# Kernel optimization log

Hardware: AMD Instinct MI355X
Metric: run time of the kernel (lower is better)

## Reference

```python
import jax, jax.numpy as jnp
import numpy as np

N_NODES = 100000


def gcn_conv(x, W, b, src, dst, n):
    """PyG GCNConv with default add_self_loops and symmetric normalization."""
    xw = x @ W  # [N, out]
    loop = jnp.arange(n, dtype=src.dtype)
    s = jnp.concatenate([src, loop])  # source j
    d = jnp.concatenate([dst, loop])  # target i
    deg = jax.ops.segment_sum(jnp.ones_like(d, dtype=xw.dtype), d, num_segments=n)
    dinv = jnp.where(deg > 0, jax.lax.rsqrt(deg), 0.0)
    norm = dinv[s] * dinv[d]  # [E+N]
    msg = xw[s] * norm[:, None]
    out = jax.ops.segment_sum(msg, d, num_segments=n)
    return out + b


def setup_inputs() -> dict:
    key = jax.random.key(0)
    ks = jax.random.split(key, 9)
    n, e, f = N_NODES, 1600000, 512
    x = jax.random.normal(ks[0], (n, f), dtype=jnp.float32)
    edge_index = jax.random.randint(ks[1], (2, e), 0, n, dtype=jnp.int32)
    y = jax.random.uniform(ks[2], (n, 1), dtype=jnp.float32)
    W1 = jax.random.normal(ks[3], (f, 64), dtype=jnp.float32) / np.sqrt(f)
    b1 = jnp.zeros((64,), jnp.float32)
    W2 = jax.random.normal(ks[4], (64, 256), dtype=jnp.float32) / np.sqrt(64)
    b2 = jnp.zeros((256,), jnp.float32)
    W3 = jax.random.normal(ks[5], (256, 1), dtype=jnp.float32) / np.sqrt(256)
    b3 = jnp.zeros((1,), jnp.float32)
    return {"x": x, "edge_index": edge_index, "y": y,
            "W1": W1, "b1": b1, "W2": W2, "b2": b2, "W3": W3, "b3": b3}


def reference(x, edge_index, y, W1, b1, W2, b2, W3, b3):
    n = x.shape[0]
    src, dst = edge_index[0], edge_index[1]
    h = jax.nn.relu(gcn_conv(x, W1, b1, src, dst, n))
    # dropout is identity in eval mode
    h = jax.nn.relu(gcn_conv(h, W2, b2, src, dst, n))
    z = gcn_conv(h, W3, b3, src, dst, n)  # logits [N, 1]
    # BCE(sigmoid(z), y), computed stably via log-sigmoid
    loss = -(y * jax.nn.log_sigmoid(z) + (1.0 - y) * jax.nn.log_sigmoid(-z))
    return jnp.mean(loss)
```

## Files before the change

### kernel.cpp

```cpp
#include <hip/hip_runtime.h>
#include <math.h>

typedef __attribute__((ext_vector_type(8))) short s16x8;
typedef __attribute__((ext_vector_type(4))) float f32x4;

__device__ inline ushort f2bf(float f) {
    union { float f; unsigned u; } v; v.f = f;
    unsigned r = v.u + 0x7FFF + ((v.u >> 16) & 1);
    return (ushort)(r >> 16);
}
__device__ inline float bf2f(ushort h) {
    union { unsigned u; float f; } v; v.u = ((unsigned)h) << 16;
    return v.f;
}
__device__ inline float bfLo(unsigned u) {
    union { unsigned x; float f; } v; v.x = u << 16; return v.f;
}
__device__ inline float bfHi(unsigned u) {
    union { unsigned x; float f; } v; v.x = u & 0xFFFF0000u; return v.f;
}


__global__ void hist_wsplit_kernel(const int* __restrict__ dst, int E, int eb,
                                   int* __restrict__ cnt8, int N, int* __restrict__ slot,
                                   const float* __restrict__ W1, const float* __restrict__ W2,
                                   ushort* __restrict__ wt_hi, ushort* __restrict__ wt_lo,
                                   ushort* __restrict__ wt2_hi, ushort* __restrict__ wt2_lo) {
    int b = blockIdx.x;
    if (b < eb) {
        int e = b * 256 + threadIdx.x;
        if (e < E) {
            int g = b & 7;
            slot[e] = atomicAdd(&cnt8[(size_t)g * N + dst[e]], 1);
        }
        return;
    }
    int idx = (b - eb) * 256 + threadIdx.x;
    if (idx < 64 * 512) {
        int n = idx & 63, k = idx >> 6;
        float f = W1[k * 64 + n];
        ushort h = f2bf(f);
        wt_hi[n * 512 + k] = h;
        wt_lo[n * 512 + k] = f2bf(f - bf2f(h));
    } else if (idx < 64 * 512 + 64 * 256) {
        int i2 = idx - 64 * 512;
        int n = i2 & 255, k = i2 >> 8;
        float f = W2[k * 256 + n];
        ushort h = f2bf(f);
        wt2_hi[n * 64 + k] = h;
        wt2_lo[n * 64 + k] = f2bf(f - bf2f(h));
    }
}

__global__ void alloc_kernel(const int* __restrict__ cnt8, int N,
                             int* __restrict__ row_start, int* __restrict__ base8,
                             int* __restrict__ deg, float* __restrict__ dinv,
                             int* __restrict__ total, float* __restrict__ out) {
    int i = blockIdx.x * blockDim.x + threadIdx.x;
    int lane = threadIdx.x & 63;
    int cg[8];
    int c = 0;
    if (i < N) {
#pragma unroll
        for (int g = 0; g < 8; g++) { cg[g] = cnt8[(size_t)g * N + i]; c += cg[g]; }
    } else {
#pragma unroll
        for (int g = 0; g < 8; g++) cg[g] = 0;
    }
    int inc = c;
#pragma unroll
    for (int o = 1; o < 64; o <<= 1) {
        int v = __shfl_up(inc, o, 64);
        if (lane >= o) inc += v;
    }
    int wsum = __shfl(inc, 63, 64);
    int base = 0;
    if (lane == 0) base = atomicAdd(total, wsum);
    base = __shfl(base, 0, 64);
    if (i < N) {
        int rs = base + inc - c;
        row_start[i] = rs;
        deg[i] = c;
        dinv[i] = rsqrtf((float)(c + 1));
        int run = rs;
#pragma unroll
        for (int g = 0; g < 8; g++) { base8[(size_t)g * N + i] = run; run += cg[g]; }
    }
    if (i == 0) *out = 0.f;
}

__global__ __launch_bounds__(256, 3) void gemm1_scatter_kernel(
        const float* __restrict__ x, const ushort* __restrict__ wt_hi,
        const ushort* __restrict__ wt_lo, const float* __restrict__ dinv,
        ushort* __restrict__ out, int N, int GB,
        const int* __restrict__ src, const int* __restrict__ dstp, int E,
        const int* __restrict__ base8, const int* __restrict__ slot,
        int* __restrict__ csr) {
    __shared__ __align__(16) short xs_hi[128 * 64];
    __shared__ __align__(16) short xs_lo[128 * 64];
    __shared__ __align__(16) short ws_hi[64 * 64];
    __shared__ __align__(16) short ws_lo[64 * 64];

    if ((int)blockIdx.x >= GB) {
        int sb = (int)blockIdx.x - GB;
        int e = sb * 256 + threadIdx.x;
        if (e < E) {
            int d = dstp[e];
            int g = sb & 7;
            csr[base8[(size_t)g * N + d] + slot[e]] = src[e];
        }
        return;
    }

    const int tid = threadIdx.x;
    const int nodeBase = blockIdx.x * 128;
    const int wave = tid >> 6, lane = tid & 63;
    const int m16 = lane & 15, quad = lane >> 4;

    f32x4 acc[2][4];
#pragma unroll
    for (int mt = 0; mt < 2; mt++)
#pragma unroll
        for (int nt = 0; nt < 4; nt++) acc[mt][nt] = (f32x4){0.f, 0.f, 0.f, 0.f};

    for (int kc = 0; kc < 512; kc += 64) {
        __syncthreads();
#pragma unroll
        for (int i = 0; i < 4; i++) {
            int f = tid + i * 256;
            int node = f >> 3, g = f & 7;
            int gn = nodeBase + node;
            if (gn >= N) gn = N - 1;
            const float4 a = *(const float4*)(x + (size_t)gn * 512 + kc + g * 8);
            const float4 b = *(const float4*)(x + (size_t)gn * 512 + kc + g * 8 + 4);
            float ff[8] = {a.x, a.y, a.z, a.w, b.x, b.y, b.z, b.w};
            union { ushort u[8]; uint4 v; } H, L;
#pragma unroll
            for (int j = 0; j < 8; j++) {
                ushort h = f2bf(ff[j]);
                H.u[j] = h;
                L.u[j] = f2bf(ff[j] - bf2f(h));
            }
            int gp = (g + node) & 7;
            *(uint4*)&xs_hi[node * 64 + gp * 8] = H.v;
            *(uint4*)&xs_lo[node * 64 + gp * 8] = L.v;
        }
#pragma unroll
        for (int i = 0; i < 2; i++) {
            int f = tid + i * 256;
            int n = f >> 3, g = f & 7;
            int gp = (g + n) & 7;
            *(uint4*)&ws_hi[n * 64 + gp * 8] =
                *(const uint4*)(wt_hi + (size_t)n * 512 + kc + g * 8);
            *(uint4*)&ws_lo[n * 64 + gp * 8] =
                *(const uint4*)(wt_lo + (size_t)n * 512 + kc + g * 8);
        }
        __syncthreads();
#pragma unroll
        for (int ck = 0; ck < 2; ck++) {
            s16x8 Ah[2], Al[2];
#pragma unroll
            for (int mt = 0; mt < 2; mt++) {
                int row = (wave * 2 + mt) * 16 + m16;
                int gp = (ck * 4 + quad + row) & 7;
                Ah[mt] = *(s16x8*)&xs_hi[row * 64 + gp * 8];
                Al[mt] = *(s16x8*)&xs_lo[row * 64 + gp * 8];
            }
#pragma unroll
            for (int nt = 0; nt < 4; nt++) {
                int n = nt * 16 + m16;
                int gp = (ck * 4 + quad + n) & 7;
                s16x8 Bh = *(s16x8*)&ws_hi[n * 64 + gp * 8];
                s16x8 Bl = *(s16x8*)&ws_lo[n * 64 + gp * 8];
#pragma unroll
                for (int mt = 0; mt < 2; mt++) {
                    acc[mt][nt] = __builtin_amdgcn_mfma_f32_16x16x32_bf16(Ah[mt], Bh, acc[mt][nt], 0, 0, 0);
                    acc[mt][nt] = __builtin_amdgcn_mfma_f32_16x16x32_bf16(Ah[mt], Bl, acc[mt][nt], 0, 0, 0);
                    acc[mt][nt] = __builtin_amdgcn_mfma_f32_16x16x32_bf16(Al[mt], Bh, acc[mt][nt], 0, 0, 0);
                }
            }
        }
    }
#pragma unroll
    for (int mt = 0; mt < 2; mt++) {
#pragma unroll
        for (int r = 0; r < 4; r++) {
            int gn = nodeBase + (wave * 2 + mt) * 16 + quad * 4 + r;
            if (gn < N) {
                float di = dinv[gn];
#pragma unroll
                for (int nt = 0; nt < 4; nt++)
                    out[(size_t)gn * 64 + nt * 16 + m16] = f2bf(di * acc[mt][nt][r]);
            }
        }
    }
}

template <int RELU, int BIAS, int PREMUL>
__global__ void agg64bf_kernel(const ushort* __restrict__ in, ushort* __restrict__ out,
                               const int* __restrict__ row_start, const int* __restrict__ deg,
                               const int* __restrict__ csr, const float* __restrict__ dinv,
                               const float* __restrict__ bias, int N) {
    int gw = (int)((blockIdx.x * (size_t)blockDim.x + threadIdx.x) >> 6);
    int lane = threadIdx.x & 63;
    if (gw >= N) return;
    const int m16 = lane & 15;
    const int quad = lane >> 4;

    const int s = row_start[gw];
    const int c = deg[gw];
    const int total = c + 1;

    float a0 = 0.f, a1 = 0.f, a2v = 0.f, a3 = 0.f;
    for (int e = 0; e < total; e += 8) {
        int s0 = e + quad, s1 = e + 4 + quad;
        bool v0 = s0 < total, v1 = s1 < total;
        int j0 = gw, j1 = gw;
        if (v0 && s0 > 0) j0 = csr[s + s0 - 1];
        if (v1 && s1 > 0) j1 = csr[s + s1 - 1];
        uint2 u0 = *(const uint2*)(in + (size_t)j0 * 64 + m16 * 4);
        uint2 u1 = *(const uint2*)(in + (size_t)j1 * 64 + m16 * 4);
        if (v0) { a0 += bfLo(u0.x); a1 += bfHi(u0.x); a2v += bfLo(u0.y); a3 += bfHi(u0.y); }
        if (v1) { a0 += bfLo(u1.x); a1 += bfHi(u1.x); a2v += bfLo(u1.y); a3 += bfHi(u1.y); }
    }
    a0 += __shfl_xor(a0, 16, 64); a0 += __shfl_xor(a0, 32, 64);
    a1 += __shfl_xor(a1, 16, 64); a1 += __shfl_xor(a1, 32, 64);
    a2v += __shfl_xor(a2v, 16, 64); a2v += __shfl_xor(a2v, 32, 64);
    a3 += __shfl_xor(a3, 16, 64); a3 += __shfl_xor(a3, 32, 64);

    float di = dinv[gw];
    float r0 = di * a0, r1 = di * a1, r2 = di * a2v, r3 = di * a3;
    if (BIAS) {
        float4 bv = *(const float4*)&bias[m16 * 4];
        r0 += bv.x; r1 += bv.y; r2 += bv.z; r3 += bv.w;
    }
    if (RELU) {
        r0 = fmaxf(r0, 0.f); r1 = fmaxf(r1, 0.f);
        r2 = fmaxf(r2, 0.f); r3 = fmaxf(r3, 0.f);
    }
    if (PREMUL) { r0 *= di; r1 *= di; r2 *= di; r3 *= di; }
    if (quad == 0) {
        uint2 o;
        o.x = ((unsigned)f2bf(r1) << 16) | f2bf(r0);
        o.y = ((unsigned)f2bf(r3) << 16) | f2bf(r2);
        *(uint2*)(out + (size_t)gw * 64 + m16 * 4) = o;
    }
}

__global__ __launch_bounds__(256, 2) void gemm23_kernel(const ushort* __restrict__ a2,
                                                        const ushort* __restrict__ wt2_hi,
                                                        const ushort* __restrict__ wt2_lo,
                                                        const float* __restrict__ b2,
                                                        const float* __restrict__ W3,
                                                        const float* __restrict__ dinv,
                                                        float* __restrict__ r, int N) {
    const int tid = threadIdx.x;
    const int wave = tid >> 6, lane = tid & 63;
    const int m16 = lane & 15, quad = lane >> 4;
    const int rowBase = blockIdx.x * 128 + wave * 32;

    s16x8 A[2][2];
#pragma unroll
    for (int mt = 0; mt < 2; mt++) {
        int gn = rowBase + mt * 16 + m16;
        if (gn >= N) gn = N - 1;
        const ushort* ap = a2 + (size_t)gn * 64 + quad * 8;
#pragma unroll
        for (int ck = 0; ck < 2; ck++)
            A[mt][ck] = *(const s16x8*)(ap + ck * 32);
    }

    f32x4 acc[2][16];
#pragma unroll
    for (int mt = 0; mt < 2; mt++)
#pragma unroll
        for (int nt = 0; nt < 16; nt++) acc[mt][nt] = (f32x4){0.f, 0.f, 0.f, 0.f};

#pragma unroll
    for (int nt = 0; nt < 16; nt++) {
        int n = nt * 16 + m16;
        const ushort* bh = wt2_hi + (size_t)n * 64 + quad * 8;
        const ushort* bl = wt2_lo + (size_t)n * 64 + quad * 8;
        s16x8 Bh0 = *(const s16x8*)(bh);
        s16x8 Bh1 = *(const s16x8*)(bh + 32);
        s16x8 Bl0 = *(const s16x8*)(bl);
        s16x8 Bl1 = *(const s16x8*)(bl + 32);
        acc[0][nt] = __builtin_amdgcn_mfma_f32_16x16x32_bf16(A[0][0], Bh0, acc[0][nt], 0, 0, 0);
        acc[1][nt] = __builtin_amdgcn_mfma_f32_16x16x32_bf16(A[1][0], Bh0, acc[1][nt], 0, 0, 0);
        acc[0][nt] = __builtin_amdgcn_mfma_f32_16x16x32_bf16(A[0][1], Bh1, acc[0][nt], 0, 0, 0);
        acc[1][nt] = __builtin_amdgcn_mfma_f32_16x16x32_bf16(A[1][1], Bh1, acc[1][nt], 0, 0, 0);
        acc[0][nt] = __builtin_amdgcn_mfma_f32_16x16x32_bf16(A[0][0], Bl0, acc[0][nt], 0, 0, 0);
        acc[1][nt] = __builtin_amdgcn_mfma_f32_16x16x32_bf16(A[1][0], Bl0, acc[1][nt], 0, 0, 0);
        acc[0][nt] = __builtin_amdgcn_mfma_f32_16x16x32_bf16(A[0][1], Bl1, acc[0][nt], 0, 0, 0);
        acc[1][nt] = __builtin_amdgcn_mfma_f32_16x16x32_bf16(A[1][1], Bl1, acc[1][nt], 0, 0, 0);
    }

    float bv[16], wv[16];
#pragma unroll
    for (int nt = 0; nt < 16; nt++) {
        bv[nt] = b2[nt * 16 + m16];
        wv[nt] = W3[nt * 16 + m16];
    }
#pragma unroll
    for (int mt = 0; mt < 2; mt++) {
#pragma unroll
        for (int rr = 0; rr < 4; rr++) {
            float p = 0.f;
#pragma unroll
            for (int nt = 0; nt < 16; nt++) {
                float v = fmaxf(acc[mt][nt][rr] + bv[nt], 0.f);
                p = fmaf(v, wv[nt], p);
            }
#pragma unroll
            for (int off = 1; off < 16; off <<= 1) p += __shfl_xor(p, off, 64);
            int gn = rowBase + mt * 16 + quad * 4 + rr;
            if (m16 == 0 && gn < N) r[gn] = dinv[gn] * p;
        }
    }
}

__global__ __launch_bounds__(1024) void loss_kernel(const float* __restrict__ r,
                                                    const float* __restrict__ dinv,
                                                    const int* __restrict__ row_start,
                                                    const int* __restrict__ deg,
                                                    const int* __restrict__ csr,
                                                    const float* __restrict__ y,
                                                    const float* __restrict__ b3,
                                                    float* __restrict__ out,
                                                    int N, float invN) {
    const int lane = threadIdx.x & 63;
    const int wave = threadIdx.x >> 6;
    const int l16 = lane & 15;
    const int grp = lane >> 4;
    const int waveId = blockIdx.x * 16 + wave;
    const int nWaves = gridDim.x * 16;
    const float b3v = b3[0];

    float loss = 0.f;
    for (int base = waveId * 4; base < N; base += nWaves * 4) {
        int node = base + grp;
        float acc = 0.f;
        if (node < N) {
            int s = row_start[node], c = deg[node];
            for (int e = l16; e < c; e += 16) acc += r[csr[s + e]];
        }
        acc += __shfl_xor(acc, 1, 64);
        acc += __shfl_xor(acc, 2, 64);
        acc += __shfl_xor(acc, 4, 64);
        acc += __shfl_xor(acc, 8, 64);
        if (node < N && l16 == 0) {
            float z = dinv[node] * (r[node] + acc) + b3v;
            float yv = y[node];
            float L = log1pf(expf(-fabsf(z)));
            float spz  = fmaxf(z, 0.f) + L;
            float spnz = fmaxf(-z, 0.f) + L;
            loss += yv * spnz + (1.f - yv) * spz;
        }
    }
#pragma unroll
    for (int off = 1; off < 64; off <<= 1) loss += __shfl_xor(loss, off, 64);
    __shared__ float red[16];
    if (lane == 0) red[wave] = loss;
    __syncthreads();
    if (threadIdx.x == 0) {
        float t = 0.f;
#pragma unroll
        for (int i = 0; i < 16; i++) t += red[i];
        atomicAdd(out, t * invN);
    }
}

extern "C" void kernel_launch(void* const* d_in, const int* in_sizes, int n_in,
                              void* d_out, int out_size, void* d_ws, size_t ws_size,
                              hipStream_t stream) {
    const float* x  = (const float*)d_in[0];
    const int*   ei = (const int*)d_in[1];
    const float* y  = (const float*)d_in[2];
    const float* W1 = (const float*)d_in[3];
    const float* b1 = (const float*)d_in[4];
    const float* W2 = (const float*)d_in[5];
    const float* b2 = (const float*)d_in[6];
    const float* W3 = (const float*)d_in[7];
    const float* b3 = (const float*)d_in[8];

    const int N = in_sizes[2];
    const int E = in_sizes[1] / 2;
    const int* src  = ei;
    const int* dstp = ei + E;

    char* w = (char*)d_ws;
    int*    cnt8      = (int*)w;    w += (size_t)8 * N * 4;
    int*    total     = (int*)w;    w += 16;
    int*    row_start = (int*)w;    w += (size_t)N * 4;
    int*    deg       = (int*)w;    w += (size_t)N * 4;
    float*  dinv      = (float*)w;  w += (size_t)N * 4;
    int*    base8     = (int*)w;    w += (size_t)8 * N * 4;
    int*    csr       = (int*)w;    w += (size_t)E * 4;
    int*    slot      = (int*)w;    w += (size_t)E * 4;
    ushort* wt_hi     = (ushort*)w; w += (size_t)64 * 512 * 2;
    ushort* wt_lo     = (ushort*)w; w += (size_t)64 * 512 * 2;
    ushort* wt2_hi    = (ushort*)w; w += (size_t)256 * 64 * 2;
    ushort* wt2_lo    = (ushort*)w; w += (size_t)256 * 64 * 2;
    ushort* pbuf      = (ushort*)w; w += (size_t)N * 64 * 2;
    ushort* qbuf      = (ushort*)w; w += (size_t)N * 64 * 2;
    float*  rbuf      = (float*)w;  w += (size_t)N * 4;

    hipMemsetAsync(cnt8, 0, (size_t)8 * N * 4 + 16, stream);

    const int tb = 256;
    const int eb = (E + tb - 1) / tb;
    const int wb = (64 * 512 + 64 * 256 + tb - 1) / tb;
    const int GB = (N + 127) / 128;

    hist_wsplit_kernel<<<eb + wb, tb, 0, stream>>>(dstp, E, eb, cnt8, N, slot,
                                                   W1, W2, wt_hi, wt_lo, wt2_hi, wt2_lo);
    alloc_kernel<<<(N + tb - 1) / tb, tb, 0, stream>>>(cnt8, N, row_start, base8, deg, dinv,
                                                       total, (float*)d_out);
    gemm1_scatter_kernel<<<GB + eb, 256, 0, stream>>>(x, wt_hi, wt_lo, dinv, pbuf, N, GB,
                                                      src, dstp, E, base8, slot, csr);
    agg64bf_kernel<1, 1, 1><<<(N + 3) / 4, 256, 0, stream>>>(pbuf, qbuf, row_start, deg, csr, dinv, b1, N);
    agg64bf_kernel<0, 0, 0><<<(N + 3) / 4, 256, 0, stream>>>(qbuf, pbuf, row_start, deg, csr, dinv, nullptr, N);

    gemm23_kernel<<<(N + 127) / 128, 256, 0, stream>>>(pbuf, wt2_hi, wt2_lo, b2, W3, dinv, rbuf, N);

    loss_kernel<<<256, 1024, 0, stream>>>(rbuf, dinv, row_start, deg, csr, y, b3,
                                          (float*)d_out, N, 1.0f / N);
}
```

Measured before the change: 605.8 us.

## Load GEMM1 operands directly into registers, bypassing LDS staging

Rewrites the first-layer GEMM so each wave loads its x rows straight from global memory into MFMA operand registers and reads the W hi/lo fragments directly from global/L2, removing the shared-memory tiles and the block-wide barriers. It also software-prefetches the next K slice of x one step ahead. The intent is to cut LDS traffic and synchronisation and to raise occupancy by freeing LDS. The risk is less coalesced global access, since each lane reads 32-byte chunks at a 2 KB row stride, and W fragments are re-read per wave instead of shared through LDS.

Measured after the change: 650.4 us. 1.07x slower.

```diff
diff --git a/kernel.cpp b/kernel.cpp
--- a/kernel.cpp
+++ b/kernel.cpp
@@ -18,6 +18,18 @@
 }
 __device__ inline float bfHi(unsigned u) {
     union { unsigned x; float f; } v; v.x = u & 0xFFFF0000u; return v.f;
+}
+
+__device__ inline void cvt8(const float4& a, const float4& b, s16x8& H, s16x8& L) {
+    float f[8] = {a.x, a.y, a.z, a.w, b.x, b.y, b.z, b.w};
+    union { ushort u[8]; s16x8 v; } hh, ll;
+#pragma unroll
+    for (int j = 0; j < 8; j++) {
+        ushort h = f2bf(f[j]);
+        hh.u[j] = h;
+        ll.u[j] = f2bf(f[j] - bf2f(h));
+    }
+    H = hh.v; L = ll.v;
 }
 
 
@@ -96,11 +108,6 @@
         const int* __restrict__ src, const int* __restrict__ dstp, int E,
         const int* __restrict__ base8, const int* __restrict__ slot,
         int* __restrict__ csr) {
-    __shared__ __align__(16) short xs_hi[128 * 64];
-    __shared__ __align__(16) short xs_lo[128 * 64];
-    __shared__ __align__(16) short ws_hi[64 * 64];
-    __shared__ __align__(16) short ws_lo[64 * 64];
-
     if ((int)blockIdx.x >= GB) {
         int sb = (int)blockIdx.x - GB;
         int e = sb * 256 + threadIdx.x;
@@ -113,9 +120,14 @@
     }
 
     const int tid = threadIdx.x;
-    const int nodeBase = blockIdx.x * 128;
     const int wave = tid >> 6, lane = tid & 63;
     const int m16 = lane & 15, quad = lane >> 4;
+    const int rowBase = blockIdx.x * 128 + wave * 32;
+
+    int gn0 = rowBase + m16;        if (gn0 >= N) gn0 = N - 1;
+    int gn1 = rowBase + 16 + m16;   if (gn1 >= N) gn1 = N - 1;
+    const float* ap0 = x + (size_t)gn0 * 512 + quad * 8;
+    const float* ap1 = x + (size_t)gn1 * 512 + quad * 8;
 
     f32x4 acc[2][4];
 #pragma unroll
@@ -123,69 +135,44 @@
 #pragma unroll
         for (int nt = 0; nt < 4; nt++) acc[mt][nt] = (f32x4){0.f, 0.f, 0.f, 0.f};
 
-    for (int kc = 0; kc < 512; kc += 64) {
-        __syncthreads();
-#pragma unroll
-        for (int i = 0; i < 4; i++) {
-            int f = tid + i * 256;
-            int node = f >> 3, g = f & 7;
-            int gn = nodeBase + node;
-            if (gn >= N) gn = N - 1;
-            const float4 a = *(const float4*)(x + (size_t)gn * 512 + kc + g * 8);
-            const float4 b = *(const float4*)(x + (size_t)gn * 512 + kc + g * 8 + 4);
-            float ff[8] = {a.x, a.y, a.z, a.w, b.x, b.y, b.z, b.w};
-            union { ushort u[8]; uint4 v; } H, L;
-#pragma unroll
-            for (int j = 0; j < 8; j++) {
-                ushort h = f2bf(ff[j]);
-                H.u[j] = h;
-                L.u[j] = f2bf(ff[j] - bf2f(h));
-            }
-            int gp = (g + node) & 7;
-            *(uint4*)&xs_hi[node * 64 + gp * 8] = H.v;
-            *(uint4*)&xs_lo[node * 64 + gp * 8] = L.v;
-        }
-#pragma unroll
-        for (int i = 0; i < 2; i++) {
-            int f = tid + i * 256;
-            int n = f >> 3, g = f & 7;
-            int gp = (g + n) & 7;
-            *(uint4*)&ws_hi[n * 64 + gp * 8] =
-                *(const uint4*)(wt_hi + (size_t)n * 512 + kc + g * 8);
-            *(uint4*)&ws_lo[n * 64 + gp * 8] =
-                *(const uint4*)(wt_lo + (size_t)n * 512 + kc + g * 8);
-        }
-        __syncthreads();
-#pragma unroll
-        for (int ck = 0; ck < 2; ck++) {
-            s16x8 Ah[2], Al[2];
-#pragma unroll
-            for (int mt = 0; mt < 2; mt++) {
-                int row = (wave * 2 + mt) * 16 + m16;
-                int gp = (ck * 4 + quad + row) & 7;
-                Ah[mt] = *(s16x8*)&xs_hi[row * 64 + gp * 8];
-                Al[mt] = *(s16x8*)&xs_lo[row * 64 + gp * 8];
-            }
-#pragma unroll
-            for (int nt = 0; nt < 4; nt++) {
-                int n = nt * 16 + m16;
-                int gp = (ck * 4 + quad + n) & 7;
-                s16x8 Bh = *(s16x8*)&ws_hi[n * 64 + gp * 8];
-                s16x8 Bl = *(s16x8*)&ws_lo[n * 64 + gp * 8];
-#pragma unroll
-                for (int mt = 0; mt < 2; mt++) {
-                    acc[mt][nt] = __builtin_amdgcn_mfma_f32_16x16x32_bf16(Ah[mt], Bh, acc[mt][nt], 0, 0, 0);
-                    acc[mt][nt] = __builtin_amdgcn_mfma_f32_16x16x32_bf16(Ah[mt], Bl, acc[mt][nt], 0, 0, 0);
-                    acc[mt][nt] = __builtin_amdgcn_mfma_f32_16x16x32_bf16(Al[mt], Bh, acc[mt][nt], 0, 0, 0);
-                }
-            }
-        }
-    }
+    float4 c0a = *(const float4*)(ap0);
+    float4 c0b = *(const float4*)(ap0 + 4);
+    float4 c1a = *(const float4*)(ap1);
+    float4 c1b = *(const float4*)(ap1 + 4);
+
+#pragma unroll
+    for (int ks = 0; ks < 16; ks++) {
+        int kn = (ks < 15) ? (ks + 1) * 32 : 15 * 32;
+        float4 n0a = *(const float4*)(ap0 + kn);
+        float4 n0b = *(const float4*)(ap0 + kn + 4);
+        float4 n1a = *(const float4*)(ap1 + kn);
+        float4 n1b = *(const float4*)(ap1 + kn + 4);
+
+        s16x8 Ah0, Al0, Ah1, Al1;
+        cvt8(c0a, c0b, Ah0, Al0);
+        cvt8(c1a, c1b, Ah1, Al1);
+
+        const int kb = ks * 32 + quad * 8;
+#pragma unroll
+        for (int nt = 0; nt < 4; nt++) {
+            int n = nt * 16 + m16;
+            s16x8 Bh = *(const s16x8*)(wt_hi + (size_t)n * 512 + kb);
+            s16x8 Bl = *(const s16x8*)(wt_lo + (size_t)n * 512 + kb);
+            acc[0][nt] = __builtin_amdgcn_mfma_f32_16x16x32_bf16(Ah0, Bh, acc[0][nt], 0, 0, 0);
+            acc[0][nt] = __builtin_amdgcn_mfma_f32_16x16x32_bf16(Ah0, Bl, acc[0][nt], 0, 0, 0);
+            acc[0][nt] = __builtin_amdgcn_mfma_f32_16x16x32_bf16(Al0, Bh, acc[0][nt], 0, 0, 0);
+            acc[1][nt] = __builtin_amdgcn_mfma_f32_16x16x32_bf16(Ah1, Bh, acc[1][nt], 0, 0, 0);
+            acc[1][nt] = __builtin_amdgcn_mfma_f32_16x16x32_bf16(Ah1, Bl, acc[1][nt], 0, 0, 0);
+            acc[1][nt] = __builtin_amdgcn_mfma_f32_16x16x32_bf16(Al1, Bh, acc[1][nt], 0, 0, 0);
+        }
+        c0a = n0a; c0b = n0b; c1a = n1a; c1b = n1b;
+    }
+
 #pragma unroll
     for (int mt = 0; mt < 2; mt++) {
 #pragma unroll
         for (int r = 0; r < 4; r++) {
-            int gn = nodeBase + (wave * 2 + mt) * 16 + quad * 4 + r;
+            int gn = rowBase + mt * 16 + quad * 4 + r;
             if (gn < N) {
                 float di = dinv[gn];
 #pragma unroll
```
